# Kernel tuning notes

Hardware: AMD Instinct MI355X
Metric: run time of the kernel (lower is better)

The kernel has to match this reference:

```python
import jax, jax.numpy as jnp
import numpy as np
import math

N_HEAD = 16
DEG = 2
EPS = 1e-7


def setup_inputs() -> dict:
    key = jax.random.key(0)
    k1, k2 = jax.random.split(key)
    B, T, C = 2, 2048, 1024
    x = jax.random.normal(k1, (B, T, C), dtype=jnp.float32)
    W = jax.random.normal(k2, (3 * C + N_HEAD, C), dtype=jnp.float32) * (1.0 / math.sqrt(C))
    return {"x": x, "W": W}


def reference(x, W):
    # JacobAttentionLayer.forward with attention_kernel='powerref' (AttentionReference,
    # deg=2, scale=1/sqrt(hs), eps=1e-7, log-space power softmax, gating=True).
    B, T, C = x.shape
    nh = N_HEAD
    hs = C // nh
    scale = 1.0 / math.sqrt(hs)

    qkvgr = jnp.einsum('btc,oc->bto', x, W)  # [B,T,3C+nh]
    q, k, v = (qkvgr[..., :C], qkvgr[..., C:2 * C], qkvgr[..., 2 * C:3 * C])
    log_g = jax.nn.log_sigmoid(qkvgr[..., 3 * C:].astype(jnp.float32))  # [B,T,nh]
    log_G = jnp.cumsum(log_g, axis=1).transpose(0, 2, 1)  # [B,nh,T]

    def heads(a):  # [B,T,C] -> [B,nh,T,hs]
        return a.reshape(B, T, nh, hs).transpose(0, 2, 1, 3)

    Q, K, V = heads(q), heads(k), heads(v)

    S = jnp.einsum('bhtd,bhsd->bhts', Q, K)  # [B,nh,T,T]
    # log-space power attention: deg*log(|S|+eps) + log(scale) + gating
    Tm = DEG * jnp.log(jnp.abs(S) + EPS) + jnp.log(jnp.float32(scale))
    Z = Tm + log_G[..., :, None] - log_G[..., None, :]
    mask = jnp.tril(jnp.ones((T, T), dtype=bool))
    Z = jnp.where(mask, Z, -jnp.inf)
    Z_rowmax = jax.lax.stop_gradient(jnp.max(Z, axis=-1, keepdims=True))
    P = jnp.exp(Z - Z_rowmax)  # deg even -> no sign correction

    norm = jnp.sum(P, axis=-1)  # [B,nh,T]
    O = jnp.einsum('bhts,bhsd->bhtd', P, V)
    y = O / norm[..., None]
    return y.transpose(0, 2, 1, 3).reshape(B, T, C)
```

## Files before the change

kernel.cpp:

```cpp
#include <hip/hip_runtime.h>
#include <math.h>

typedef __attribute__((ext_vector_type(4))) float f32x4;
typedef __attribute__((ext_vector_type(8))) short short8;

#define NEG_INF (-__builtin_inff())

__device__ __forceinline__ unsigned short f2bf(float f) {
    union { float f; unsigned u; } v; v.f = f;
    unsigned r = v.u + 0x7FFFu + ((v.u >> 16) & 1u);
    return (unsigned short)(r >> 16);
}
__device__ __forceinline__ unsigned short f2bf_trunc(float f) {
    union { float f; unsigned u; } v; v.f = f;
    return (unsigned short)(v.u >> 16);
}
__device__ __forceinline__ float bf2f(unsigned short h) {
    union { unsigned u; float f; } v; v.u = ((unsigned)h) << 16;
    return v.f;
}

__device__ __forceinline__ f32x4 mfma_bf16(short8 a, short8 b, f32x4 c) {
    return __builtin_amdgcn_mfma_f32_16x16x32_bf16(a, b, c, 0, 0, 0);
}

__device__ __forceinline__ void gload_lds16(const unsigned short* g, unsigned short* l) {
    __builtin_amdgcn_global_load_lds(
        (const __attribute__((address_space(1))) void*)g,
        (__attribute__((address_space(3))) void*)l, 16, 0, 0);
}

__global__ void split_kernel(const float* __restrict__ in,
                             unsigned short* __restrict__ hi,
                             unsigned short* __restrict__ lo, int n4)
{
    int i = blockIdx.x * 256 + threadIdx.x;
    if (i >= n4) return;
    float4 v = ((const float4*)in)[i];
    ushort4 h, l;
    h.x = f2bf(v.x); l.x = f2bf(v.x - bf2f(h.x));
    h.y = f2bf(v.y); l.y = f2bf(v.y - bf2f(h.y));
    h.z = f2bf(v.z); l.z = f2bf(v.z - bf2f(h.z));
    h.w = f2bf(v.w); l.w = f2bf(v.w - bf2f(h.w));
    ((ushort4*)hi)[i] = h;
    ((ushort4*)lo)[i] = l;
}

__global__ __launch_bounds__(256, 2)
void gemm_proj(const unsigned short* __restrict__ xh, const unsigned short* __restrict__ xl,
               const unsigned short* __restrict__ wh, const unsigned short* __restrict__ wl,
               unsigned short* __restrict__ Qh, unsigned short* __restrict__ Ql,
               unsigned short* __restrict__ Kh, unsigned short* __restrict__ Kl,
               unsigned short* __restrict__ Vtg, float* __restrict__ gbuf)
{
    __shared__ __align__(16) unsigned short Ah[2][128][32];
    __shared__ __align__(16) unsigned short Al[2][128][32];
    __shared__ __align__(16) unsigned short Bh[2][128][32];
    __shared__ __align__(16) unsigned short Bl[2][128][32];

    const int mt = blockIdx.x & 31;
    const int nt = blockIdx.x >> 5;
    const int m0 = mt * 128, n0 = nt * 128;
    const int tid = threadIdx.x;
    const int w = tid >> 6, l = tid & 63;
    const int wm = w >> 1, wn = w & 1;
    const int lr = l & 15, lq = l >> 4;
    const int xs = (lr >> 1) & 3;
    const bool needLo = (nt < 16) || (nt == 24);

    f32x4 acc[4][4];
#pragma unroll
    for (int i = 0; i < 4; ++i)
#pragma unroll
        for (int j = 0; j < 4; ++j) acc[i][j] = (f32x4){0.f, 0.f, 0.f, 0.f};

    const int srow = tid >> 2;
    const int sp = tid & 3;

    auto STAGE = [&](int bsel, int k0) {
#pragma unroll
        for (int p = 0; p < 2; ++p) {
            int r = srow + p * 64;
            int sc = (sp ^ ((r >> 1) & 3)) * 8;
            int o = n0 + r;
            int oc = o < 3088 ? o : 3087;
            gload_lds16(&xh[(size_t)(m0 + r) * 1024 + k0 + sc], &Ah[bsel][r][sp * 8]);
            gload_lds16(&wh[(size_t)oc * 1024 + k0 + sc],       &Bh[bsel][r][sp * 8]);
            if (needLo) {
                gload_lds16(&xl[(size_t)(m0 + r) * 1024 + k0 + sc], &Al[bsel][r][sp * 8]);
                gload_lds16(&wl[(size_t)oc * 1024 + k0 + sc],       &Bl[bsel][r][sp * 8]);
            }
        }
    };

    STAGE(0, 0);
    __asm__ volatile("s_waitcnt vmcnt(0)" ::: "memory");
    __syncthreads();

    int cur = 0;
    for (int k0 = 0; k0 < 1024; k0 += 32) {
        if (k0 + 32 < 1024) STAGE(cur ^ 1, k0 + 32);

        short8 ah[4], bh4[4], al4[4], bl4[4];
#pragma unroll
        for (int i = 0; i < 4; ++i) {
            ah[i]  = *(const short8*)&Ah[cur][wm * 64 + i * 16 + lr][(lq ^ xs) * 8];
            bh4[i] = *(const short8*)&Bh[cur][wn * 64 + i * 16 + lr][(lq ^ xs) * 8];
        }
        if (needLo) {
#pragma unroll
            for (int i = 0; i < 4; ++i) {
                al4[i] = *(const short8*)&Al[cur][wm * 64 + i * 16 + lr][(lq ^ xs) * 8];
                bl4[i] = *(const short8*)&Bl[cur][wn * 64 + i * 16 + lr][(lq ^ xs) * 8];
            }
        }
#pragma unroll
        for (int i = 0; i < 4; ++i)
#pragma unroll
            for (int j = 0; j < 4; ++j) {
                acc[i][j] = mfma_bf16(ah[i], bh4[j], acc[i][j]);
                if (needLo) {
                    acc[i][j] = mfma_bf16(ah[i], bl4[j], acc[i][j]);
                    acc[i][j] = mfma_bf16(al4[i], bh4[j], acc[i][j]);
                }
            }

        __asm__ volatile("s_waitcnt vmcnt(0)" ::: "memory");
        __syncthreads();
        cur ^= 1;
    }

#pragma unroll
    for (int i = 0; i < 4; ++i) {
        int nrow0 = m0 + wm * 64 + i * 16 + lq * 4;
        int b = nrow0 >> 11;
        int tbase = nrow0 & 2047;
#pragma unroll
        for (int j = 0; j < 4; ++j) {
            int o = n0 + wn * 64 + j * 16 + lr;
            if (o < 1024) {
                int h = o >> 6, d = o & 63;
                size_t base = ((size_t)(b * 16 + h) * 2048 + tbase) * 64 + d;
#pragma unroll
                for (int r = 0; r < 4; ++r) {
                    float v = acc[i][j][r];
                    unsigned short hi_ = f2bf(v);
                    unsigned short lo_ = f2bf(v - bf2f(hi_));
                    Qh[base + (size_t)r * 64] = hi_;
                    Ql[base + (size_t)r * 64] = lo_;
                }
            } else if (o < 2048) {
                int oo = o - 1024;
                int h = oo >> 6, d = oo & 63;
                size_t base = ((size_t)(b * 16 + h) * 2048 + tbase) * 64 + d;
#pragma unroll
                for (int r = 0; r < 4; ++r) {
                    float v = acc[i][j][r];
                    unsigned short hi_ = f2bf(v);
                    unsigned short lo_ = f2bf(v - bf2f(hi_));
                    Kh[base + (size_t)r * 64] = hi_;
                    Kl[base + (size_t)r * 64] = lo_;
                }
            } else if (o < 3072) {
                int oo = o - 2048;
                int h = oo >> 6, d = oo & 63;
                size_t base = ((size_t)(b * 16 + h) * 64 + d) * 2048 + tbase;
                ushort4 pk;
                pk.x = f2bf(acc[i][j][0]);
                pk.y = f2bf(acc[i][j][1]);
                pk.z = f2bf(acc[i][j][2]);
                pk.w = f2bf(acc[i][j][3]);
                *(ushort4*)&Vtg[base] = pk;
            } else if (o < 3088) {
                int og = o - 3072;
#pragma unroll
                for (int r = 0; r < 4; ++r)
                    gbuf[(size_t)(nrow0 + r) * 16 + og] = acc[i][j][r];
            }
        }
    }
}

__global__ void gate_scan(const float* __restrict__ g, float* __restrict__ lg)
{
    const int bh = blockIdx.x;
    const int b = bh >> 4, h = bh & 15;
    const int tid = threadIdx.x;
    __shared__ float part[256];

    float vals[8];
    float run = 0.f;
#pragma unroll
    for (int j = 0; j < 8; ++j) {
        int t = tid * 8 + j;
        float x = g[(size_t)(b * 2048 + t) * 16 + h];
        float ls = fminf(x, 0.f) - log1pf(__expf(-fabsf(x)));
        run += ls * 1.4426950408889634f;
        vals[j] = run;
    }
    part[tid] = run;
    __syncthreads();
    for (int ofs = 1; ofs < 256; ofs <<= 1) {
        float add = (tid >= ofs) ? part[tid - ofs] : 0.f;
        __syncthreads();
        part[tid] += add;
        __syncthreads();
    }
    float excl = part[tid] - run;
#pragma unroll
    for (int j = 0; j < 8; ++j)
        lg[(size_t)bh * 2048 + tid * 8 + j] = excl + vals[j];
}

__global__ __launch_bounds__(256, 3)
void attn_fwd(const unsigned short* __restrict__ Qh, const unsigned short* __restrict__ Ql,
              const unsigned short* __restrict__ Kh, const unsigned short* __restrict__ Kl,
              const unsigned short* __restrict__ Vtg, const float* __restrict__ lg,
              float* __restrict__ out)
{
    __shared__ __align__(16) unsigned short kh[2][64][64];
    __shared__ __align__(16) unsigned short kl[2][64][64];
    __shared__ __align__(16) unsigned short pl[4][16][64];

    const int bid = blockIdx.x;
    const int x8 = bid & 7;
    const int k  = bid >> 3;
    const int m  = k >> 2;
    const int bh = x8 + 8 * (k & 3);
    const int qi = (m & 1) ? (31 - (m >> 1)) : (m >> 1);
    const int tid = threadIdx.x;
    const int w = tid >> 6, l = tid & 63;
    const int lr = l & 15, lq = l >> 4;
    const int xk = lr & 7;
    const int q0 = qi * 64;
    const int myrow0 = q0 + w * 16;

    const size_t qoff = ((size_t)bh * 2048 + myrow0 + lr) * 64;
    short8 qh8[2], ql8[2];
    qh8[0] = *(const short8*)&Qh[qoff + lq * 8];
    qh8[1] = *(const short8*)&Qh[qoff + 32 + lq * 8];
    ql8[0] = *(const short8*)&Ql[qoff + lq * 8];
    ql8[1] = *(const short8*)&Ql[qoff + 32 + lq * 8];

    float gq2[4];
#pragma unroll
    for (int r = 0; r < 4; ++r)
        gq2[r] = lg[(size_t)bh * 2048 + myrow0 + lq * 4 + r] - 3.0f;

    f32x4 ls4 = (f32x4){0.f, 0.f, 0.f, 0.f};
    f32x4 o4[4];
#pragma unroll
    for (int i = 0; i < 4; ++i) o4[i] = (f32x4){0.f, 0.f, 0.f, 0.f};

    short8 ones8;
#pragma unroll
    for (int j = 0; j < 8; ++j) ones8[j] = (short)0x3F80;

    const int srow = tid >> 3;
    const int schunk = tid & 7;

    const unsigned short* Kh_b = Kh + (size_t)bh * 2048 * 64;
    const unsigned short* Kl_b = Kl + (size_t)bh * 2048 * 64;
    const unsigned short* Vt_b = Vtg + (size_t)bh * 64 * 2048;

    auto STAGE = [&](int bsel, int kv0) {
#pragma unroll
        for (int p = 0; p < 2; ++p) {
            int r = srow + p * 32;
            int sc = (schunk ^ (r & 7)) * 8;
            gload_lds16(&Kh_b[(size_t)(kv0 + r) * 64 + sc], &kh[bsel][r][schunk * 8]);
            gload_lds16(&Kl_b[(size_t)(kv0 + r) * 64 + sc], &kl[bsel][r][schunk * 8]);
        }
    };

    STAGE(0, 0);
    __asm__ volatile("s_waitcnt vmcnt(0)" ::: "memory");
    __syncthreads();

    int cur = 0;
    for (int kv0 = 0; kv0 <= q0; kv0 += 64) {
        uint4 vreg[8];
#pragma unroll
        for (int ds_ = 0; ds_ < 4; ++ds_) {
            const unsigned short* vp = &Vt_b[(size_t)(ds_ * 16 + lr) * 2048 + kv0 + lq * 8];
            vreg[ds_ * 2]     = *(const uint4*)vp;
            vreg[ds_ * 2 + 1] = *(const uint4*)(vp + 32);
        }
        if (kv0 + 64 <= q0) STAGE(cur ^ 1, kv0 + 64);

        float gsl[4];
#pragma unroll
        for (int js = 0; js < 4; ++js)
            gsl[js] = lg[(size_t)bh * 2048 + kv0 + js * 16 + lr];

        f32x4 sa[4];
#pragma unroll
        for (int js = 0; js < 4; ++js) sa[js] = (f32x4){0.f, 0.f, 0.f, 0.f};
#pragma unroll
        for (int js = 0; js < 4; ++js)
#pragma unroll
            for (int ks = 0; ks < 2; ++ks) {
                short8 kb  = *(const short8*)&kh[cur][js * 16 + lr][((ks * 4 + lq) ^ xk) << 3];
                short8 kbl = *(const short8*)&kl[cur][js * 16 + lr][((ks * 4 + lq) ^ xk) << 3];
                sa[js] = mfma_bf16(qh8[ks], kb,  sa[js]);
                sa[js] = mfma_bf16(qh8[ks], kbl, sa[js]);
                sa[js] = mfma_bf16(ql8[ks], kb,  sa[js]);
            }

        const bool diag = (kv0 == q0);
#pragma unroll
        for (int js = 0; js < 4; ++js) {
            float ga = gsl[js];
#pragma unroll
            for (int r = 0; r < 4; ++r) {
                float a = fabsf(sa[js][r]) + 1e-7f;
                float ex = exp2f(gq2[r] - ga);
                float wv = a * a * ex;
                if (diag && (js * 16 + lr > w * 16 + lq * 4 + r)) wv = 0.f;
                sa[js][r] = wv;
            }
        }

#pragma unroll
        for (int js = 0; js < 4; ++js)
#pragma unroll
            for (int r = 0; r < 4; ++r) {
                int prow = lq * 4 + r;
                int cch = (js * 2 + (lr >> 3)) ^ (prow & 7);
                pl[w][prow][(cch << 3) | (lr & 7)] = f2bf_trunc(sa[js][r]);
            }
        __asm__ volatile("s_waitcnt lgkmcnt(0)" ::: "memory");
        __builtin_amdgcn_sched_barrier(0);

        short8 pa0 = *(const short8*)&pl[w][lr][((0 + lq) ^ xk) << 3];
        short8 pa1 = *(const short8*)&pl[w][lr][((4 + lq) ^ xk) << 3];

        ls4 = mfma_bf16(pa0, ones8, ls4);
        ls4 = mfma_bf16(pa1, ones8, ls4);
#pragma unroll
        for (int ds_ = 0; ds_ < 4; ++ds_) {
            short8 vb0 = *(const short8*)&vreg[ds_ * 2];
            short8 vb1 = *(const short8*)&vreg[ds_ * 2 + 1];
            o4[ds_] = mfma_bf16(pa0, vb0, o4[ds_]);
            o4[ds_] = mfma_bf16(pa1, vb1, o4[ds_]);
        }

        __asm__ volatile("s_waitcnt vmcnt(0)" ::: "memory");
        __syncthreads();
        cur ^= 1;
    }

    const int b = bh >> 4, h = bh & 15;
#pragma unroll
    for (int ds_ = 0; ds_ < 4; ++ds_)
#pragma unroll
        for (int r = 0; r < 4; ++r) {
            int t = myrow0 + lq * 4 + r;
            out[(size_t)(b * 2048 + t) * 1024 + h * 64 + ds_ * 16 + lr] =
                o4[ds_][r] / ls4[r];
        }
}

extern "C" void kernel_launch(void* const* d_in, const int* in_sizes, int n_in,
                              void* d_out, int out_size, void* d_ws, size_t ws_size,
                              hipStream_t stream)
{
    const float* x = (const float*)d_in[0];
    const float* W = (const float*)d_in[1];
    float* out = (float*)d_out;

    const size_t NX = 4194304;
    const size_t NW = 3162112;
    const size_t NQ = 4194304;

    char* ws = (char*)d_ws;
    size_t off = 0;
    auto alloc = [&](size_t bytes) -> void* {
        void* p = ws + off;
        off += (bytes + 255) & ~(size_t)255;
        return p;
    };
    unsigned short* xh = (unsigned short*)alloc(NX * 2);
    unsigned short* xl = (unsigned short*)alloc(NX * 2);
    unsigned short* wh = (unsigned short*)alloc(NW * 2);
    unsigned short* wl = (unsigned short*)alloc(NW * 2);
    unsigned short* Qh = (unsigned short*)alloc(NQ * 2);
    unsigned short* Ql = (unsigned short*)alloc(NQ * 2);
    unsigned short* Kh = (unsigned short*)alloc(NQ * 2);
    unsigned short* Kl = (unsigned short*)alloc(NQ * 2);
    unsigned short* Vt = (unsigned short*)alloc(NQ * 2);
    float* g  = (float*)alloc(65536 * 4);
    float* lg = (float*)alloc(65536 * 4);
    if (off > ws_size) return;

    split_kernel<<<(int)(NX / 4 + 255) / 256, 256, 0, stream>>>(x, xh, xl, (int)(NX / 4));
    split_kernel<<<(int)(NW / 4 + 255) / 256, 256, 0, stream>>>(W, wh, wl, (int)(NW / 4));
    gemm_proj<<<800, 256, 0, stream>>>(xh, xl, wh, wl, Qh, Ql, Kh, Kl, Vt, g);
    gate_scan<<<32, 256, 0, stream>>>(g, lg);
    attn_fwd<<<1024, 256, 0, stream>>>(Qh, Ql, Kh, Kl, Vt, lg, out);
}
```

Baseline: 200.0 us.

## Process two 64-row query groups per block to reuse staged K/V tiles

Each attention block now handles 128 query rows as two 64-row groups sharing the same K/V tile loads, which halves the grid to 512 blocks and changes the causal tile scheduling. The aim is to halve K/V global and LDS traffic per query row. It raises register use, so launch bounds drop to 2 blocks per SIMD, and it adds a branch that skips the lower group on the final diagonal tile. Fewer blocks and lower occupancy may hurt latency hiding and load balance.

```diff
diff --git a/kernel.cpp b/kernel.cpp
--- a/kernel.cpp
+++ b/kernel.cpp
@@ -3,8 +3,6 @@
 
 typedef __attribute__((ext_vector_type(4))) float f32x4;
 typedef __attribute__((ext_vector_type(8))) short short8;
-
-#define NEG_INF (-__builtin_inff())
 
 __device__ __forceinline__ unsigned short f2bf(float f) {
     union { float f; unsigned u; } v; v.f = f;
@@ -212,7 +210,7 @@
         lg[(size_t)bh * 2048 + tid * 8 + j] = excl + vals[j];
 }
 
-__global__ __launch_bounds__(256, 3)
+__global__ __launch_bounds__(256, 2)
 void attn_fwd(const unsigned short* __restrict__ Qh, const unsigned short* __restrict__ Ql,
               const unsigned short* __restrict__ Kh, const unsigned short* __restrict__ Kl,
               const unsigned short* __restrict__ Vtg, const float* __restrict__ lg,
@@ -220,37 +218,42 @@
 {
     __shared__ __align__(16) unsigned short kh[2][64][64];
     __shared__ __align__(16) unsigned short kl[2][64][64];
-    __shared__ __align__(16) unsigned short pl[4][16][64];
+    __shared__ __align__(16) unsigned short pl[2][4][16][64];
 
     const int bid = blockIdx.x;
     const int x8 = bid & 7;
     const int k  = bid >> 3;
+    const int bh = x8 + 8 * (k & 3);
     const int m  = k >> 2;
-    const int bh = x8 + 8 * (k & 3);
-    const int qi = (m & 1) ? (31 - (m >> 1)) : (m >> 1);
+    const int qi = (m < 8) ? m : 23 - m;
     const int tid = threadIdx.x;
     const int w = tid >> 6, l = tid & 63;
     const int lr = l & 15, lq = l >> 4;
     const int xk = lr & 7;
-    const int q0 = qi * 64;
-    const int myrow0 = q0 + w * 16;
-
-    const size_t qoff = ((size_t)bh * 2048 + myrow0 + lr) * 64;
-    short8 qh8[2], ql8[2];
-    qh8[0] = *(const short8*)&Qh[qoff + lq * 8];
-    qh8[1] = *(const short8*)&Qh[qoff + 32 + lq * 8];
-    ql8[0] = *(const short8*)&Ql[qoff + lq * 8];
-    ql8[1] = *(const short8*)&Ql[qoff + 32 + lq * 8];
-
-    float gq2[4];
-#pragma unroll
-    for (int r = 0; r < 4; ++r)
-        gq2[r] = lg[(size_t)bh * 2048 + myrow0 + lq * 4 + r] - 3.0f;
-
-    f32x4 ls4 = (f32x4){0.f, 0.f, 0.f, 0.f};
-    f32x4 o4[4];
-#pragma unroll
-    for (int i = 0; i < 4; ++i) o4[i] = (f32x4){0.f, 0.f, 0.f, 0.f};
+    const int q0 = qi * 128;
+
+    short8 qh8[2][2], ql8[2][2];
+    float gq2[2][4];
+#pragma unroll
+    for (int g = 0; g < 2; ++g) {
+        const size_t qoff = ((size_t)bh * 2048 + q0 + g * 64 + w * 16 + lr) * 64;
+        qh8[g][0] = *(const short8*)&Qh[qoff + lq * 8];
+        qh8[g][1] = *(const short8*)&Qh[qoff + 32 + lq * 8];
+        ql8[g][0] = *(const short8*)&Ql[qoff + lq * 8];
+        ql8[g][1] = *(const short8*)&Ql[qoff + 32 + lq * 8];
+#pragma unroll
+        for (int r = 0; r < 4; ++r)
+            gq2[g][r] = lg[(size_t)bh * 2048 + q0 + g * 64 + w * 16 + lq * 4 + r] - 3.0f;
+    }
+
+    f32x4 ls4[2];
+    f32x4 o4[2][4];
+#pragma unroll
+    for (int g = 0; g < 2; ++g) {
+        ls4[g] = (f32x4){0.f, 0.f, 0.f, 0.f};
+#pragma unroll
+        for (int i = 0; i < 4; ++i) o4[g][i] = (f32x4){0.f, 0.f, 0.f, 0.f};
+    }
 
     short8 ones8;
 #pragma unroll
@@ -277,8 +280,9 @@
     __asm__ volatile("s_waitcnt vmcnt(0)" ::: "memory");
     __syncthreads();
 
+    const int kvmax = q0 + 64;
     int cur = 0;
-    for (int kv0 = 0; kv0 <= q0; kv0 += 64) {
+    for (int kv0 = 0; kv0 <= kvmax; kv0 += 64) {
         uint4 vreg[8];
 #pragma unroll
         for (int ds_ = 0; ds_ < 4; ++ds_) {
@@ -286,63 +290,74 @@
             vreg[ds_ * 2]     = *(const uint4*)vp;
             vreg[ds_ * 2 + 1] = *(const uint4*)(vp + 32);
         }
-        if (kv0 + 64 <= q0) STAGE(cur ^ 1, kv0 + 64);
+        if (kv0 < kvmax) STAGE(cur ^ 1, kv0 + 64);
 
         float gsl[4];
 #pragma unroll
         for (int js = 0; js < 4; ++js)
             gsl[js] = lg[(size_t)bh * 2048 + kv0 + js * 16 + lr];
 
-        f32x4 sa[4];
-#pragma unroll
-        for (int js = 0; js < 4; ++js) sa[js] = (f32x4){0.f, 0.f, 0.f, 0.f};
+        const bool g0on = (kv0 <= q0);
+        const bool d0 = (kv0 == q0);
+        const bool d1 = (kv0 == kvmax);
+
+        f32x4 sa[2][4];
+#pragma unroll
+        for (int g = 0; g < 2; ++g)
+#pragma unroll
+            for (int js = 0; js < 4; ++js) sa[g][js] = (f32x4){0.f, 0.f, 0.f, 0.f};
 #pragma unroll
         for (int js = 0; js < 4; ++js)
 #pragma unroll
             for (int ks = 0; ks < 2; ++ks) {
                 short8 kb  = *(const short8*)&kh[cur][js * 16 + lr][((ks * 4 + lq) ^ xk) << 3];
                 short8 kbl = *(const short8*)&kl[cur][js * 16 + lr][((ks * 4 + lq) ^ xk) << 3];
-                sa[js] = mfma_bf16(qh8[ks], kb,  sa[js]);
-                sa[js] = mfma_bf16(qh8[ks], kbl, sa[js]);
-                sa[js] = mfma_bf16(ql8[ks], kb,  sa[js]);
-            }
-
-        const bool diag = (kv0 == q0);
-#pragma unroll
-        for (int js = 0; js < 4; ++js) {
-            float ga = gsl[js];
-#pragma unroll
-            for (int r = 0; r < 4; ++r) {
-                float a = fabsf(sa[js][r]) + 1e-7f;
-                float ex = exp2f(gq2[r] - ga);
-                float wv = a * a * ex;
-                if (diag && (js * 16 + lr > w * 16 + lq * 4 + r)) wv = 0.f;
-                sa[js][r] = wv;
-            }
-        }
-
-#pragma unroll
-        for (int js = 0; js < 4; ++js)
-#pragma unroll
-            for (int r = 0; r < 4; ++r) {
-                int prow = lq * 4 + r;
-                int cch = (js * 2 + (lr >> 3)) ^ (prow & 7);
-                pl[w][prow][(cch << 3) | (lr & 7)] = f2bf_trunc(sa[js][r]);
-            }
+                if (g0on) {
+                    sa[0][js] = mfma_bf16(qh8[0][ks], kb,  sa[0][js]);
+                    sa[0][js] = mfma_bf16(qh8[0][ks], kbl, sa[0][js]);
+                    sa[0][js] = mfma_bf16(ql8[0][ks], kb,  sa[0][js]);
+                }
+                sa[1][js] = mfma_bf16(qh8[1][ks], kb,  sa[1][js]);
+                sa[1][js] = mfma_bf16(qh8[1][ks], kbl, sa[1][js]);
+                sa[1][js] = mfma_bf16(ql8[1][ks], kb,  sa[1][js]);
+            }
+
+#pragma unroll
+        for (int g = 0; g < 2; ++g) {
+            if (g == 0 && !g0on) continue;
+            const bool dg = g ? d1 : d0;
+#pragma unroll
+            for (int js = 0; js < 4; ++js) {
+                float ga = gsl[js];
+#pragma unroll
+                for (int r = 0; r < 4; ++r) {
+                    float a = fabsf(sa[g][js][r]) + 1e-7f;
+                    float ex = exp2f(gq2[g][r] - ga);
+                    float wv = a * a * ex;
+                    if (dg && (js * 16 + lr > w * 16 + lq * 4 + r)) wv = 0.f;
+                    int prow = lq * 4 + r;
+                    int cch = (js * 2 + (lr >> 3)) ^ (prow & 7);
+                    pl[g][w][prow][(cch << 3) | (lr & 7)] = f2bf_trunc(wv);
+                }
+            }
+        }
         __asm__ volatile("s_waitcnt lgkmcnt(0)" ::: "memory");
         __builtin_amdgcn_sched_barrier(0);
 
-        short8 pa0 = *(const short8*)&pl[w][lr][((0 + lq) ^ xk) << 3];
-        short8 pa1 = *(const short8*)&pl[w][lr][((4 + lq) ^ xk) << 3];
-
-        ls4 = mfma_bf16(pa0, ones8, ls4);
-        ls4 = mfma_bf16(pa1, ones8, ls4);
-#pragma unroll
-        for (int ds_ = 0; ds_ < 4; ++ds_) {
-            short8 vb0 = *(const short8*)&vreg[ds_ * 2];
-            short8 vb1 = *(const short8*)&vreg[ds_ * 2 + 1];
-            o4[ds_] = mfma_bf16(pa0, vb0, o4[ds_]);
-            o4[ds_] = mfma_bf16(pa1, vb1, o4[ds_]);
+#pragma unroll
+        for (int g = 0; g < 2; ++g) {
+            if (g == 0 && !g0on) continue;
+            short8 pa0 = *(const short8*)&pl[g][w][lr][((0 + lq) ^ xk) << 3];
+            short8 pa1 = *(const short8*)&pl[g][w][lr][((4 + lq) ^ xk) << 3];
+            ls4[g] = mfma_bf16(pa0, ones8, ls4[g]);
+            ls4[g] = mfma_bf16(pa1, ones8, ls4[g]);
+#pragma unroll
+            for (int ds_ = 0; ds_ < 4; ++ds_) {
+                short8 vb0 = *(const short8*)&vreg[ds_ * 2];
+                short8 vb1 = *(const short8*)&vreg[ds_ * 2 + 1];
+                o4[g][ds_] = mfma_bf16(pa0, vb0, o4[g][ds_]);
+                o4[g][ds_] = mfma_bf16(pa1, vb1, o4[g][ds_]);
+            }
         }
 
         __asm__ volatile("s_waitcnt vmcnt(0)" ::: "memory");
@@ -352,13 +367,15 @@
 
     const int b = bh >> 4, h = bh & 15;
 #pragma unroll
-    for (int ds_ = 0; ds_ < 4; ++ds_)
-#pragma unroll
-        for (int r = 0; r < 4; ++r) {
-            int t = myrow0 + lq * 4 + r;
-            out[(size_t)(b * 2048 + t) * 1024 + h * 64 + ds_ * 16 + lr] =
-                o4[ds_][r] / ls4[r];
-        }
+    for (int g = 0; g < 2; ++g)
+#pragma unroll
+        for (int ds_ = 0; ds_ < 4; ++ds_)
+#pragma unroll
+            for (int r = 0; r < 4; ++r) {
+                int t = q0 + g * 64 + w * 16 + lq * 4 + r;
+                out[(size_t)(b * 2048 + t) * 1024 + h * 64 + ds_ * 16 + lr] =
+                    o4[g][ds_][r] / ls4[g][r];
+            }
 }
 
 extern "C" void kernel_launch(void* const* d_in, const int* in_sizes, int n_in,
@@ -397,5 +414,5 @@
     split_kernel<<<(int)(NW / 4 + 255) / 256, 256, 0, stream>>>(W, wh, wl, (int)(NW / 4));
     gemm_proj<<<800, 256, 0, stream>>>(xh, xl, wh, wl, Qh, Ql, Kh, Kl, Vt, g);
     gate_scan<<<32, 256, 0, stream>>>(g, lg);
-    attn_fwd<<<1024, 256, 0, stream>>>(Qh, Ql, Kh, Kl, Vt, lg, out);
-}
+    attn_fwd<<<512, 256, 0, stream>>>(Qh, Ql, Kh, Kl, Vt, lg, out);
+}
```

Result: slower. 205.8 us (+2.9%).
